# Performance work log

Measured on AMD Instinct MI355X. Metric: run time of the kernel, lower is better.

## Reference

```python
import jax, jax.numpy as jnp
import numpy as np

LEAKY_SLOPE = 0.01  # torch nn.LeakyReLU default


def leaky_relu(x):
    return jnp.where(x >= 0, x, LEAKY_SLOPE * x)


def rgcn_conv(x, edge_index, edge_type, w_rel, w_root, b_conv):
    # PyG RGCNConv: out = x @ W_root + b + sum_r mean_{edges of rel r into i}(x_src @ W_r)
    n = x.shape[0]
    src, dst = edge_index[0], edge_index[1]
    out = x @ w_root + b_conv
    num_rel = w_rel.shape[0]
    for r in range(num_rel):  # small fixed relation count
        mask = (edge_type == r)
        msg = x[src] @ w_rel[r]                      # [E, H]
        msg = jnp.where(mask[:, None], msg, 0.0)
        agg = jax.ops.segment_sum(msg, dst, num_segments=n)          # [N, H]
        cnt = jax.ops.segment_sum(mask.astype(x.dtype), dst, num_segments=n)
        out = out + agg / jnp.maximum(cnt, 1.0)[:, None]             # mean aggr
    return out


def setup_inputs() -> dict:
    key = jax.random.key(0)
    ks = jax.random.split(key, 10)
    N, E, D_IN, H, OUT, R = 50000, 600000, 768, 128, 3, 2
    s_in = 1.0 / np.sqrt(D_IN)
    s_h = 1.0 / np.sqrt(H)
    return {
        "feature": jax.random.normal(ks[0], (N, D_IN), dtype=jnp.float32),
        "edge_index": jax.random.randint(ks[1], (2, E), 0, N, dtype=jnp.int64),
        "edge_type": jax.random.randint(ks[2], (E,), 0, R, dtype=jnp.int64),
        "w_in": jax.random.uniform(ks[3], (D_IN, H), jnp.float32, -s_in, s_in),
        "b_in": jax.random.uniform(ks[4], (H,), jnp.float32, -s_in, s_in),
        "w_rel": jax.random.uniform(ks[5], (R, H, H), jnp.float32, -s_h, s_h),
        "w_root": jax.random.uniform(ks[6], (H, H), jnp.float32, -s_h, s_h),
        "b_conv": jnp.zeros((H,), jnp.float32),
        "w_out": jax.random.uniform(ks[7], (H, OUT), jnp.float32, -s_h, s_h),
        "b_out": jax.random.uniform(ks[8], (OUT,), jnp.float32, -s_h, s_h),
    }


def reference(feature, edge_index, edge_type, w_in, b_in, w_rel, w_root, b_conv, w_out, b_out):
    x = leaky_relu(feature @ w_in + b_in)
    # NOTE: original forward applies rgcn1 twice (shared weights); dropout is
    # identity at inference; rgcn2/linear_relu_output1 are unused.
    x = rgcn_conv(x, edge_index, edge_type, w_rel, w_root, b_conv)
    x = rgcn_conv(x, edge_index, edge_type, w_rel, w_root, b_conv)
    return x @ w_out + b_out
```

## Files before the change

kernel.cpp:

```cpp
#include <hip/hip_runtime.h>

#define H 128
#define CAP 64

typedef _Float16 f16x8 __attribute__((ext_vector_type(8)));
typedef float    f32x4 __attribute__((ext_vector_type(4)));

__global__ __launch_bounds__(256) void prep_all(const float* __restrict__ w_in,
    const float* __restrict__ w_root, const float* __restrict__ w_rel,
    const float* __restrict__ b_conv, const float* __restrict__ w_out,
    const float* __restrict__ b_out, _Float16* __restrict__ wInT,
    _Float16* __restrict__ wcatT, float* __restrict__ wfin,
    float* __restrict__ bfin, int K, int OUT)
{
    int idx = blockIdx.x * 256 + threadIdx.x;
    int tot1 = K * H;
    if (idx < tot1) {
        int k = idx >> 7, c = idx & 127;
        int o = ((k >> 3) << 10) + (c << 3) + (k & 7);
        wInT[o] = (_Float16)w_in[idx];
        return;
    }
    int i2 = idx - tot1;
    if (i2 < H * 384) {
        int c = i2 / 384, k = i2 - c * 384;
        float v;
        if (k < 128)      v = w_root[(size_t)k * H + c];
        else if (k < 256) v = w_rel[(size_t)(k - 128) * H + c];
        else              v = w_rel[(size_t)H * H + (size_t)(k - 256) * H + c];
        wcatT[i2] = (_Float16)v;
        return;
    }
    int i3 = i2 - H * 384;
    int nw = 3 * H * OUT;
    if (i3 < nw) {
        int mk = i3 / OUT, c = i3 - mk * OUT;
        int m = mk >> 7, k = mk & 127;
        const float* W = (m == 0) ? w_root : (w_rel + (size_t)(m - 1) * H * H);
        float s = 0.f;
        for (int j = 0; j < H; j++)
            s += W[(size_t)k * H + j] * w_out[(size_t)j * OUT + c];
        wfin[(size_t)mk * OUT + c] = s;
    } else if (i3 < nw + OUT) {
        int c = i3 - nw;
        float s = b_out[c];
        for (int j = 0; j < H; j++) s += b_conv[j] * w_out[(size_t)j * OUT + c];
        bfin[c] = s;
    }
}

__device__ __forceinline__ f16x8 cvt8(float4 v0, float4 v1) {
    f16x8 t;
    t[0] = (_Float16)v0.x; t[1] = (_Float16)v0.y; t[2] = (_Float16)v0.z; t[3] = (_Float16)v0.w;
    t[4] = (_Float16)v1.x; t[5] = (_Float16)v1.y; t[6] = (_Float16)v1.z; t[7] = (_Float16)v1.w;
    return t;
}

__global__ __launch_bounds__(256, 2) void gemm_hist(const float* __restrict__ A,
    const _Float16* __restrict__ WP, const float* __restrict__ bias,
    _Float16* __restrict__ C16, int M, int K, int ldc, int gemmBlocks,
    const int* __restrict__ esrc, const int* __restrict__ edst,
    const int* __restrict__ et, int* __restrict__ cnt, int* __restrict__ elist,
    int E, int N)
{
    __shared__ float As[2][4][2048];

    if ((int)blockIdx.x >= gemmBlocks) {
        int e = (blockIdx.x - gemmBlocks) * 256 + threadIdx.x;
        if (e < E) {
            int s = esrc[e], d = edst[e], t = et[e];
            int b = t * N + d;
            int pos = atomicAdd(&cnt[b], 1);
            if (pos < CAP)
                __builtin_nontemporal_store(s, &elist[(size_t)b * CAP + pos]);
        }
        return;
    }

    const int tid = threadIdx.x;
    const int w   = tid >> 6;
    const int l   = tid & 63;
    const int l15 = l & 15;
    const int q   = l >> 4;
    const int brow = blockIdx.x * 64;
    const int wr   = w * 16;

    const int lh  = l >> 5;
    const int l31 = l & 31;

    const _Float16* bp = WP + ((size_t)q * H + l15) * 8;

    float bj[8];
#pragma unroll
    for (int j = 0; j < 8; j++) bj[j] = bias[j * 16 + l15];

    f32x4 acc[8];
    const f32x4 z4 = {0.f, 0.f, 0.f, 0.f};
#pragma unroll
    for (int j = 0; j < 8; j++) acc[j] = z4;

    const int chunks = K / 128;

#define STAGE(c, nbuf)                                                          \
    {                                                                           \
        _Pragma("unroll")                                                       \
        for (int i = 0; i < 8; i++) {                                           \
            int r  = 2 * i + lh;                                                \
            int gr = brow + wr + r; if (gr >= M) gr = M - 1;                    \
            int cg = l31 ^ (r & 7);                                             \
            const float* ga = A + (size_t)gr * K + (c) * 128 + cg * 4;          \
            __builtin_amdgcn_global_load_lds(                                   \
                (const __attribute__((address_space(1))) void*)ga,              \
                (__attribute__((address_space(3))) void*)&As[nbuf][w][i * 256], \
                16, 0, 0);                                                      \
        }                                                                       \
    }

    STAGE(0, 0);
    __syncthreads();

    for (int c = 0; c < chunks; c++) {
        if (c + 1 < chunks) STAGE(c + 1, (c + 1) & 1);

        const float* wbuf = As[c & 1][w];
#pragma unroll
        for (int ks = 0; ks < 4; ks++) {
            const int sl = ks * 4 + q;
            const int xr = l15 & 7;
            const int p0 = (2 * sl) ^ xr;
            const int p1 = (2 * sl + 1) ^ xr;
            float4 lo = *(const float4*)&wbuf[l15 * 128 + p0 * 4];
            float4 hi = *(const float4*)&wbuf[l15 * 128 + p1 * 4];
            f16x8 af = cvt8(lo, hi);
            const _Float16* bks = bp + (size_t)(c * 4 + ks) * 4096;
            f16x8 bf[8];
#pragma unroll
            for (int j = 0; j < 8; j++) bf[j] = *(const f16x8*)(bks + j * 128);
#pragma unroll
            for (int j = 0; j < 8; j++)
                acc[j] = __builtin_amdgcn_mfma_f32_16x16x32_f16(af, bf[j], acc[j], 0, 0, 0);
        }
        __syncthreads();
    }
#undef STAGE

#pragma unroll
    for (int rg = 0; rg < 4; rg++) {
        int row = brow + wr + q * 4 + rg;
        if (row < M) {
#pragma unroll
            for (int j = 0; j < 8; j++) {
                float v = acc[j][rg] + bj[j];
                v = (v >= 0.f) ? v : 0.01f * v;
                C16[(size_t)row * ldc + j * 16 + l15] = (_Float16)v;
            }
        }
    }
}

__global__ __launch_bounds__(256) void fused_l1(const _Float16* __restrict__ X1,
    const _Float16* __restrict__ WT, const float* __restrict__ bias,
    const int* __restrict__ elist, const int* __restrict__ cnt,
    _Float16* __restrict__ X2, int N)
{
    __shared__ _Float16 Ml[16][264];

    const int w   = threadIdx.x >> 6;
    const int l   = threadIdx.x & 63;
    const int l15 = l & 15;
    const int q   = l >> 4;
    const int r0  = blockIdx.x * 16;

    const int eo   = l >> 4;
    const int e2   = eo & 1;
    const int half = l >> 5;
    const int c8   = l15 * 8;

    const f16x8 zv = {};
#pragma unroll
    for (int i = 0; i < 4; i++) {
        const int rl = w * 4 + i;
        const int r  = r0 + rl;
        float acc[8];
#pragma unroll
        for (int j = 0; j < 8; j++) acc[j] = 0.f;
        float inv = 0.f;
        if (r < N) {
            int dr = cnt[(size_t)half * N + r];
            int d  = dr < CAP ? dr : CAP;
            inv = dr > 0 ? 1.f / (float)dr : 0.f;
            const int* lst = elist + ((size_t)half * N + r) * CAP;
            for (int p = e2; p < d; p += 8) {
                int p1 = p + 2, p2 = p + 4, p3 = p + 6;
                int s0 = lst[p];
                f16x8 v0 = *(const f16x8*)&X1[(size_t)s0 * H + c8];
                f16x8 v1 = zv, v2 = zv, v3 = zv;
                if (p1 < d) { int s = lst[p1]; v1 = *(const f16x8*)&X1[(size_t)s * H + c8]; }
                if (p2 < d) { int s = lst[p2]; v2 = *(const f16x8*)&X1[(size_t)s * H + c8]; }
                if (p3 < d) { int s = lst[p3]; v3 = *(const f16x8*)&X1[(size_t)s * H + c8]; }
#pragma unroll
                for (int j = 0; j < 8; j++)
                    acc[j] += (float)v0[j] + (float)v1[j] + (float)v2[j] + (float)v3[j];
            }
        }
#pragma unroll
        for (int j = 0; j < 8; j++) {
            acc[j] += __shfl_xor(acc[j], 16);
            acc[j] *= inv;
        }
        if (r < N && (eo == 0 || eo == 2)) {
            f16x8 o;
#pragma unroll
            for (int j = 0; j < 8; j++) o[j] = (_Float16)acc[j];
            *(f16x8*)&Ml[rl][half * 128 + c8] = o;
        }
    }
    __syncthreads();

    int gr = r0 + l15; if (gr >= N) gr = N - 1;
    f16x8 xf[12];
    {
        const _Float16* xp = X1 + (size_t)gr * H + q * 8;
#pragma unroll
        for (int c = 0; c < 4; c++) xf[c] = *(const f16x8*)(xp + c * 32);
#pragma unroll
        for (int c = 4; c < 12; c++) xf[c] = *(const f16x8*)&Ml[l15][(c - 4) * 32 + q * 8];
    }

    const f32x4 z4 = {0.f, 0.f, 0.f, 0.f};
#pragma unroll
    for (int cf = 0; cf < 2; cf++) {
        const int col = w * 32 + cf * 16 + l15;
        f16x8 bf[12];
        const _Float16* wpp = WT + (size_t)col * 384 + q * 8;
#pragma unroll
        for (int c = 0; c < 12; c++) bf[c] = *(const f16x8*)(wpp + c * 32);
        f32x4 a0 = z4;
#pragma unroll
        for (int c = 0; c < 12; c++)
            a0 = __builtin_amdgcn_mfma_f32_16x16x32_f16(xf[c], bf[c], a0, 0, 0, 0);
        const float bj = bias[col];
#pragma unroll
        for (int rg = 0; rg < 4; rg++) {
            int row = r0 + q * 4 + rg;
            if (row < N) X2[(size_t)row * H + col] = (_Float16)(a0[rg] + bj);
        }
    }
}

template<int MODE>
__global__ __launch_bounds__(256) void gather_k(const _Float16* __restrict__ X,
    int ldx, _Float16* __restrict__ Mout, const int* __restrict__ elist,
    const int* __restrict__ cnt, int N,
    const float* __restrict__ wfin, const float* __restrict__ bfin,
    float* __restrict__ out)
{
    int wv = blockIdx.x * 4 + (threadIdx.x >> 6);
    int l  = threadIdx.x & 63;
    if (wv >= N) return;

    const int eo   = l >> 4;
    const int e2   = eo & 1;
    const int half = l >> 5;
    const int c8   = (l & 15) * 8;

    int dr = cnt[(size_t)half * N + wv];
    int d  = dr < CAP ? dr : CAP;
    float inv = dr > 0 ? 1.f / (float)dr : 0.f;
    const int* lst = elist + ((size_t)half * N + wv) * CAP;

    float acc[8];
#pragma unroll
    for (int j = 0; j < 8; j++) acc[j] = 0.f;

    const f16x8 zv = {};
    for (int p = e2; p < d; p += 8) {
        int p1 = p + 2, p2 = p + 4, p3 = p + 6;
        int s0 = lst[p];
        f16x8 v0 = *(const f16x8*)&X[(size_t)s0 * ldx + c8];
        f16x8 v1 = zv, v2 = zv, v3 = zv;
        if (p1 < d) { int s = lst[p1]; v1 = *(const f16x8*)&X[(size_t)s * ldx + c8]; }
        if (p2 < d) { int s = lst[p2]; v2 = *(const f16x8*)&X[(size_t)s * ldx + c8]; }
        if (p3 < d) { int s = lst[p3]; v3 = *(const f16x8*)&X[(size_t)s * ldx + c8]; }
#pragma unroll
        for (int j = 0; j < 8; j++)
            acc[j] += (float)v0[j] + (float)v1[j] + (float)v2[j] + (float)v3[j];
    }

#pragma unroll
    for (int j = 0; j < 8; j++) {
        acc[j] += __shfl_xor(acc[j], 16);
        acc[j] *= inv;
    }

    if (MODE == 0) {
        if (eo == 0 || eo == 2) {
            f16x8 o;
#pragma unroll
            for (int j = 0; j < 8; j++) o[j] = (_Float16)acc[j];
            *(f16x8*)&Mout[(size_t)wv * 256 + half * 128 + c8] = o;
        }
    } else {
        float p0 = 0.f, p1 = 0.f, p2 = 0.f;
        if (eo == 1) {
            f16x8 xv = *(const f16x8*)&X[(size_t)wv * ldx + c8];
#pragma unroll
            for (int j = 0; j < 8; j++) {
                float xf = (float)xv[j];
                const float* wr = wfin + (size_t)(c8 + j) * 3;
                p0 += xf * wr[0]; p1 += xf * wr[1]; p2 += xf * wr[2];
            }
        } else if (eo == 0 || eo == 2) {
            const float* wb = wfin + (size_t)(eo == 0 ? 1 : 2) * H * 3;
#pragma unroll
            for (int j = 0; j < 8; j++) {
                const float* wr = wb + (size_t)(c8 + j) * 3;
                p0 += acc[j] * wr[0]; p1 += acc[j] * wr[1]; p2 += acc[j] * wr[2];
            }
        }
#pragma unroll
        for (int off = 1; off <= 32; off <<= 1) {
            p0 += __shfl_xor(p0, off);
            p1 += __shfl_xor(p1, off);
            p2 += __shfl_xor(p2, off);
        }
        if (l == 0) {
            out[(size_t)wv * 3 + 0] = p0 + bfin[0];
            out[(size_t)wv * 3 + 1] = p1 + bfin[1];
            out[(size_t)wv * 3 + 2] = p2 + bfin[2];
        }
    }
}

__global__ __launch_bounds__(512) void gemm_cat(const _Float16* __restrict__ X1,
    const _Float16* __restrict__ Mt, const _Float16* __restrict__ WT,
    const float* __restrict__ bias, _Float16* __restrict__ X2, int M, int mtiles)
{
    const int w   = threadIdx.x >> 6;
    const int l   = threadIdx.x & 63;
    const int l15 = l & 15;
    const int q   = l >> 4;
    const int col = w * 16 + l15;

    f16x8 bf[12];
    {
        const _Float16* wpp = WT + (size_t)col * 384 + q * 8;
#pragma unroll
        for (int c = 0; c < 12; c++) bf[c] = *(const f16x8*)(wpp + c * 32);
    }
    const float bj = bias[col];

    int t = blockIdx.x;
    if (t >= mtiles) return;
    f16x8 xf[12];
    {
        const _Float16* xp = X1 + ((size_t)t * 16 + l15) * 128 + q * 8;
        const _Float16* mp = Mt + ((size_t)t * 16 + l15) * 256 + q * 8;
#pragma unroll
        for (int c = 0; c < 4; c++) xf[c] = *(const f16x8*)(xp + c * 32);
#pragma unroll
        for (int c = 4; c < 12; c++) xf[c] = *(const f16x8*)(mp + (c - 4) * 32);
    }

    const f32x4 z4 = {0.f, 0.f, 0.f, 0.f};
    while (true) {
        int tn = t + gridDim.x;
        bool more = tn < mtiles;
        f16x8 xnf[12];
        if (more) {
            const _Float16* xp = X1 + ((size_t)tn * 16 + l15) * 128 + q * 8;
            const _Float16* mp = Mt + ((size_t)tn * 16 + l15) * 256 + q * 8;
#pragma unroll
            for (int c = 0; c < 4; c++) xnf[c] = *(const f16x8*)(xp + c * 32);
#pragma unroll
            for (int c = 4; c < 12; c++) xnf[c] = *(const f16x8*)(mp + (c - 4) * 32);
        }

        f32x4 a0 = z4;
#pragma unroll
        for (int c = 0; c < 12; c++)
            a0 = __builtin_amdgcn_mfma_f32_16x16x32_f16(xf[c], bf[c], a0, 0, 0, 0);

#pragma unroll
        for (int rg = 0; rg < 4; rg++) {
            int row = t * 16 + q * 4 + rg;
            if (row < M) X2[(size_t)row * 128 + col] = (_Float16)(a0[rg] + bj);
        }
        if (!more) break;
        t = tn;
#pragma unroll
        for (int c = 0; c < 12; c++) xf[c] = xnf[c];
    }
}

__global__ __launch_bounds__(256) void proj_generic(const _Float16* __restrict__ X2,
    const _Float16* __restrict__ Mt, const float* __restrict__ wfin,
    const float* __restrict__ bfin, float* __restrict__ out, int N, int OUT)
{
    int row = blockIdx.x * 4 + (threadIdx.x >> 6);
    int l = threadIdx.x & 63;
    if (row >= N) return;
    float xv[6];
#pragma unroll
    for (int i = 0; i < 6; i++) {
        int k = l * 6 + i;
        xv[i] = (k < 128) ? (float)X2[(size_t)row * 128 + k]
                          : (float)Mt[(size_t)row * 256 + (k - 128)];
    }
    for (int c = 0; c < OUT; c++) {
        float p = 0.f;
#pragma unroll
        for (int i = 0; i < 6; i++) p += xv[i] * wfin[(size_t)(l * 6 + i) * OUT + c];
        for (int off = 32; off > 0; off >>= 1) p += __shfl_down(p, off);
        if (l == 0) out[(size_t)row * OUT + c] = p + bfin[c];
    }
}

extern "C" void kernel_launch(void* const* d_in, const int* in_sizes, int n_in,
                              void* d_out, int out_size, void* d_ws, size_t ws_size,
                              hipStream_t stream) {
    const float* feature = (const float*)d_in[0];
    const int*   ei      = (const int*)d_in[1];
    const int*   et      = (const int*)d_in[2];
    const float* w_in    = (const float*)d_in[3];
    const float* b_in    = (const float*)d_in[4];
    const float* w_rel   = (const float*)d_in[5];
    const float* w_root  = (const float*)d_in[6];
    const float* b_conv  = (const float*)d_in[7];
    const float* w_out   = (const float*)d_in[8];
    const float* b_out   = (const float*)d_in[9];

    const int HH   = in_sizes[4];
    const int D_IN = in_sizes[3] / HH;
    const int N    = in_sizes[0] / D_IN;
    const int E    = in_sizes[1] / 2;
    const int OUT  = in_sizes[9];

    char* base = (char*)d_ws;
    _Float16* wInT  = (_Float16*)base;
    _Float16* wcatT = wInT + (size_t)D_IN * HH;
    _Float16* X1    = wcatT + (size_t)HH * 384;
    _Float16* X2    = X1 + (size_t)N * HH;
    _Float16* Mt    = X2 + (size_t)N * HH;
    float* wfin     = (float*)(Mt + (size_t)N * 256);
    float* bfin     = wfin + (size_t)3 * HH * (OUT > 0 ? OUT : 1);
    int* cnt        = (int*)(bfin + ((OUT + 3) & ~3));
    int* elist      = cnt + (size_t)2 * N;

    hipMemsetAsync(cnt, 0, sizeof(int) * (size_t)2 * N, stream);
    {
        int ptot = D_IN * HH + HH * 384 + 3 * HH * OUT + OUT;
        prep_all<<<(ptot + 255) / 256, 256, 0, stream>>>(
            w_in, w_root, w_rel, b_conv, w_out, b_out,
            wInT, wcatT, wfin, bfin, D_IN, OUT);
    }

    const int gemmBlocks = (N + 63) / 64;
    const int histBlocks = (E + 255) / 256;
    gemm_hist<<<gemmBlocks + histBlocks, 256, 0, stream>>>(
        feature, wInT, b_in, X1, N, D_IN, HH, gemmBlocks,
        ei, ei + E, et, cnt, elist, E, N);

    const int mtiles  = (N + 15) / 16;
    const int gblocks = (N + 3) / 4;

    if (OUT == 3) {
        fused_l1<<<mtiles, 256, 0, stream>>>(X1, wcatT, b_conv, elist, cnt, X2, N);
        gather_k<1><<<gblocks, 256, 0, stream>>>(X2, 128, nullptr, elist, cnt, N,
                                                 wfin, bfin, (float*)d_out);
    } else {
        gather_k<0><<<gblocks, 256, 0, stream>>>(X1, 128, Mt, elist, cnt, N,
                                                 nullptr, nullptr, nullptr);
        gemm_cat<<<1024, 512, 0, stream>>>(X1, Mt, wcatT, b_conv, X2, N, mtiles);
        gather_k<0><<<gblocks, 256, 0, stream>>>(X2, 128, Mt, elist, cnt, N,
                                                 nullptr, nullptr, nullptr);
        proj_generic<<<gblocks, 256, 0, stream>>>(X2, Mt, wfin, bfin,
                                                  (float*)d_out, N, OUT);
    }
}
```

Measured before the change: 398.7 us.

## Project layer-2 features to output dims before gathering neighbors

Because the mean aggregation and the final linear projection are both linear, each node's 128-wide fp16 feature is first projected to 9 floats (root plus two relation projections), and the per-edge gather then reads these small 12-float rows instead of 128-wide feature rows. This removes most of the gather bandwidth in the last layer. The cost is an extra kernel launch and an N×12 float intermediate, and the gather now runs one thread per node, which gives less parallelism per node and uncoalesced 16-byte reads.

```diff
diff --git a/kernel.cpp b/kernel.cpp
--- a/kernel.cpp
+++ b/kernel.cpp
@@ -4,6 +4,7 @@
 #define CAP 64
 
 typedef _Float16 f16x8 __attribute__((ext_vector_type(8)));
+typedef _Float16 f16x2 __attribute__((ext_vector_type(2)));
 typedef float    f32x4 __attribute__((ext_vector_type(4)));
 
 __global__ __launch_bounds__(256) void prep_all(const float* __restrict__ w_in,
@@ -248,6 +249,82 @@
     }
 }
 
+__global__ __launch_bounds__(256) void proj9(const _Float16* __restrict__ X2,
+    const float* __restrict__ wfin, float* __restrict__ P, int N)
+{
+    int row = blockIdx.x * 4 + (threadIdx.x >> 6);
+    int l   = threadIdx.x & 63;
+    if (row >= N) return;
+
+    f16x2 xv = *(const f16x2*)&X2[(size_t)row * H + 2 * l];
+    float x0 = (float)xv[0], x1 = (float)xv[1];
+
+    float p[9];
+#pragma unroll
+    for (int c = 0; c < 9; c++) {
+        int m  = (c < 3) ? 1 : (c < 6) ? 2 : 0;
+        int cc = (c < 3) ? c : (c < 6) ? c - 3 : c - 6;
+        float w0 = wfin[(size_t)(m * H + 2 * l) * 3 + cc];
+        float w1 = wfin[(size_t)(m * H + 2 * l + 1) * 3 + cc];
+        p[c] = x0 * w0 + x1 * w1;
+    }
+#pragma unroll
+    for (int off = 1; off <= 32; off <<= 1)
+#pragma unroll
+        for (int c = 0; c < 9; c++) p[c] += __shfl_xor(p[c], off);
+
+    if (l == 0) {
+        float* pr = P + (size_t)row * 12;
+#pragma unroll
+        for (int c = 0; c < 3; c++) {
+            pr[c]     = p[c];
+            pr[4 + c] = p[3 + c];
+            pr[8 + c] = p[6 + c];
+        }
+    }
+}
+
+__global__ __launch_bounds__(256) void gather_fin(const float* __restrict__ P,
+    const int* __restrict__ elist, const int* __restrict__ cnt,
+    const float* __restrict__ bfin, float* __restrict__ out, int N)
+{
+    int i = blockIdx.x * 256 + threadIdx.x;
+    if (i >= N) return;
+
+    float o0 = P[(size_t)i * 12 + 8] + bfin[0];
+    float o1 = P[(size_t)i * 12 + 9] + bfin[1];
+    float o2 = P[(size_t)i * 12 + 10] + bfin[2];
+
+#pragma unroll
+    for (int r = 0; r < 2; r++) {
+        int dr = cnt[(size_t)r * N + i];
+        int d  = dr < CAP ? dr : CAP;
+        float inv = dr > 0 ? 1.f / (float)dr : 0.f;
+        const int* lst = elist + ((size_t)r * N + i) * CAP;
+        float s0 = 0.f, s1 = 0.f, s2 = 0.f;
+        int p = 0;
+        for (; p + 3 < d; p += 4) {
+            int a = lst[p], b = lst[p + 1], c = lst[p + 2], e = lst[p + 3];
+            float4 va = *(const float4*)&P[(size_t)a * 12 + r * 4];
+            float4 vb = *(const float4*)&P[(size_t)b * 12 + r * 4];
+            float4 vc = *(const float4*)&P[(size_t)c * 12 + r * 4];
+            float4 ve = *(const float4*)&P[(size_t)e * 12 + r * 4];
+            s0 += va.x + vb.x + vc.x + ve.x;
+            s1 += va.y + vb.y + vc.y + ve.y;
+            s2 += va.z + vb.z + vc.z + ve.z;
+        }
+        for (; p < d; p++) {
+            int a = lst[p];
+            float4 va = *(const float4*)&P[(size_t)a * 12 + r * 4];
+            s0 += va.x; s1 += va.y; s2 += va.z;
+        }
+        o0 += s0 * inv; o1 += s1 * inv; o2 += s2 * inv;
+    }
+    out[(size_t)i * 3 + 0] = o0;
+    out[(size_t)i * 3 + 1] = o1;
+    out[(size_t)i * 3 + 2] = o2;
+}
+
 template<int MODE>
 __global__ __launch_bounds__(256) void gather_k(const _Float16* __restrict__ X,
     int ldx, _Float16* __restrict__ Mout, const int* __restrict__ elist,
@@ -299,35 +376,6 @@
 #pragma unroll
             for (int j = 0; j < 8; j++) o[j] = (_Float16)acc[j];
             *(f16x8*)&Mout[(size_t)wv * 256 + half * 128 + c8] = o;
-        }
-    } else {
-        float p0 = 0.f, p1 = 0.f, p2 = 0.f;
-        if (eo == 1) {
-            f16x8 xv = *(const f16x8*)&X[(size_t)wv * ldx + c8];
-#pragma unroll
-            for (int j = 0; j < 8; j++) {
-                float xf = (float)xv[j];
-                const float* wr = wfin + (size_t)(c8 + j) * 3;
-                p0 += xf * wr[0]; p1 += xf * wr[1]; p2 += xf * wr[2];
-            }
-        } else if (eo == 0 || eo == 2) {
-            const float* wb = wfin + (size_t)(eo == 0 ? 1 : 2) * H * 3;
-#pragma unroll
-            for (int j = 0; j < 8; j++) {
-                const float* wr = wb + (size_t)(c8 + j) * 3;
-                p0 += acc[j] * wr[0]; p1 += acc[j] * wr[1]; p2 += acc[j] * wr[2];
-            }
-        }
-#pragma unroll
-        for (int off = 1; off <= 32; off <<= 1) {
-            p0 += __shfl_xor(p0, off);
-            p1 += __shfl_xor(p1, off);
-            p2 += __shfl_xor(p2, off);
-        }
-        if (l == 0) {
-            out[(size_t)wv * 3 + 0] = p0 + bfin[0];
-            out[(size_t)wv * 3 + 1] = p1 + bfin[1];
-            out[(size_t)wv * 3 + 2] = p2 + bfin[2];
         }
     }
 }
@@ -442,7 +490,8 @@
     _Float16* X1    = wcatT + (size_t)HH * 384;
     _Float16* X2    = X1 + (size_t)N * HH;
     _Float16* Mt    = X2 + (size_t)N * HH;
-    float* wfin     = (float*)(Mt + (size_t)N * 256);
+    float* Pt       = (float*)(Mt + (size_t)N * 256);
+    float* wfin     = Pt + (size_t)N * 12;
     float* bfin     = wfin + (size_t)3 * HH * (OUT > 0 ? OUT : 1);
     int* cnt        = (int*)(bfin + ((OUT + 3) & ~3));
     int* elist      = cnt + (size_t)2 * N;
@@ -466,8 +515,9 @@
 
     if (OUT == 3) {
         fused_l1<<<mtiles, 256, 0, stream>>>(X1, wcatT, b_conv, elist, cnt, X2, N);
-        gather_k<1><<<gblocks, 256, 0, stream>>>(X2, 128, nullptr, elist, cnt, N,
-                                                 wfin, bfin, (float*)d_out);
+        proj9<<<gblocks, 256, 0, stream>>>(X2, wfin, Pt, N);
+        gather_fin<<<(N + 255) / 256, 256, 0, stream>>>(Pt, elist, cnt, bfin,
+                                                        (float*)d_out, N);
     } else {
         gather_k<0><<<gblocks, 256, 0, stream>>>(X1, 128, Mt, elist, cnt, N,
                                                  nullptr, nullptr, nullptr);
```

Result: no change. 401.2 us (+0.6%).
